# Kernel optimization log

Measured on AMD Instinct MI355X. Metric: run time of the kernel, lower is better.

Reference implementation:

```python
import jax, jax.numpy as jnp
import numpy as np

K = 5      # kernel_size
STRIDE = 1
EPS = 1e-7


def _extract_patches(x, k, s):
    # x: [B,H,W,C] -> [B,Ho,Wo,k,k,C], same (kh,kw,c) layout as tf.extract_image_patches VALID
    B, H, W, C = x.shape
    Ho = (H - k) // s + 1
    Wo = (W - k) // s + 1
    r = (jnp.arange(Ho) * s)[:, None] + jnp.arange(k)   # [Ho,k]
    c = (jnp.arange(Wo) * s)[:, None] + jnp.arange(k)   # [Wo,k]
    return x[:, r[:, None, :, None], c[None, :, None, :], :]


def _rotate(pflat, angle, k):
    # Replicates tf.contrib.image.transform with angles_to_projective_transforms,
    # including the (1+1e-7) normalization of the 3x3 matrix in the original code.
    # pflat: [N, k*k, C], angle: [N]; bilinear sampling, fill value 0 outside.
    N = pflat.shape[0]
    f32 = pflat.dtype
    co, si = jnp.cos(angle), jnp.sin(angle)
    km1 = jnp.asarray(k - 1, f32)
    xoff = (km1 - (co * km1 - si * km1)) * 0.5
    yoff = (km1 - (si * km1 + co * km1)) * 0.5
    scale = 1.0 / (1.0 + EPS)  # transforms /= transforms[:, 8:9] + 1e-7
    gy, gx = jnp.meshgrid(jnp.arange(k, dtype=f32), jnp.arange(k, dtype=f32), indexing='ij')
    sx = (co[:, None, None] * gx - si[:, None, None] * gy + xoff[:, None, None]) * scale
    sy = (si[:, None, None] * gx + co[:, None, None] * gy + yoff[:, None, None]) * scale
    sx = sx.reshape(N, k * k)
    sy = sy.reshape(N, k * k)
    x0 = jnp.floor(sx)
    y0 = jnp.floor(sy)
    wx = (sx - x0)[..., None]
    wy = (sy - y0)[..., None]
    x0i = x0.astype(jnp.int32)
    y0i = y0.astype(jnp.int32)

    def samp(yi, xi):
        valid = (xi >= 0) & (xi < k) & (yi >= 0) & (yi < k)
        idx = jnp.clip(yi, 0, k - 1) * k + jnp.clip(xi, 0, k - 1)   # [N,k*k]
        v = jnp.take_along_axis(pflat, idx[..., None], axis=1)      # [N,k*k,C]
        return jnp.where(valid[..., None], v, jnp.zeros((), f32))

    v00 = samp(y0i, x0i)
    v01 = samp(y0i, x0i + 1)
    v10 = samp(y0i + 1, x0i)
    v11 = samp(y0i + 1, x0i + 1)
    top = v00 * (1 - wx) + v01 * wx
    bot = v10 * (1 - wx) + v11 * wx
    return top * (1 - wy) + bot * wy   # [N,k*k,C]


def _forward(input_tensor, W, b):
    k, s = K, STRIDE
    B, H, Wd, C = input_tensor.shape
    patches = _extract_patches(input_tensor, k, s)      # [B,Ho,Wo,k,k,C]
    Ho, Wo = patches.shape[1], patches.shape[2]
    inten = patches.sum(-1)                             # [B,Ho,Wo,k,k] channel-sum intensity
    ridx = jnp.arange(k, dtype=patches.dtype)
    tot = inten.sum((-2, -1)) + EPS
    cr = (inten * ridx[:, None]).sum((-2, -1)) / tot    # centroid row
    cc = (inten * ridx[None, :]).sum((-2, -1)) / tot    # centroid col
    m = (k - 1) / 2.0                                   # meanCenter (same for row/col)
    angle = jnp.arctan2(cr - m, cc - m + EPS)           # [B,Ho,Wo]
    pflat = patches.reshape(B * Ho * Wo, k * k, C)
    rot = _rotate(pflat, angle.reshape(-1), k)          # [N,k*k,C]
    rot = rot.reshape(B, Ho * Wo, k * k * C)
    wflat = W.reshape(W.shape[0], -1)                   # [F, k*k*C]
    out = jnp.einsum('bpd,fd->bpf', rot, wflat)         # elementwise-mult-sum 'conv'
    return out.reshape(B, Ho, Wo, -1) + b


def setup_inputs():
    key = jax.random.key(0)
    k1, k2 = jax.random.split(key, 2)
    B, H, Wd, C, F = 4, 128, 128, 16, 32
    input_tensor = jax.random.uniform(k1, (B, H, Wd, C), dtype=jnp.float32)
    lim = float(np.sqrt(6.0 / (K * K * C + F)))  # glorot_uniform
    W = jax.random.uniform(k2, (F, K, K, C), minval=-lim, maxval=lim, dtype=jnp.float32)
    b = jnp.zeros((F,), jnp.float32)
    return {"input_tensor": input_tensor, "W": W, "b": b}


def reference(input_tensor, W, b):
    return _forward(input_tensor, W, b)
```

## Files before the change

### kernel.cpp

```cpp
#include <hip/hip_runtime.h>


#define KS     5
#define TILE   8
#define TW     (TILE + KS - 1)
#define SINH   24
#define C_IN   16
#define F_OUT  32
#define H_IN   128
#define W_IN   128
#define HO     124
#define WO     124
#define NBATCH 4
#define EPSF   1e-7f
#define BLOCK  256
#define KW     400

#define PART_OFF    6912
#define ANG_OFF     9216
#define RED_STRIDE  34
#define RED_WAVE    (64 * RED_STRIDE)
#define SMEM_BYTES  34816

typedef _Float16 half8  __attribute__((ext_vector_type(8)));
typedef _Float16 half4v __attribute__((ext_vector_type(4)));
typedef __attribute__((ext_vector_type(4))) float floatx4;

static __device__ __forceinline__ half8 blend8h(
    const _Float16* __restrict__ s_inh, int lxq, int lyq,
    float co, float si, float xo, float yo, int t, int ch0)
{
    const float scl = 1.0f / (1.0f + EPSF);
    int ky = t / KS, kx = t - KS * ky;
    float sx = (co * (float)kx - si * (float)ky + xo) * scl;
    float sy = (si * (float)kx + co * (float)ky + yo) * scl;
    float fx0 = floorf(sx), fy0 = floorf(sy);
    float wx = sx - fx0, wy = sy - fy0;
    int x0 = (int)fx0, y0 = (int)fy0;
    int x1 = x0 + 1, y1 = y0 + 1;
    float vx0 = (x0 >= 0 && x0 < KS) ? 1.f : 0.f;
    float vx1 = (x1 >= 0 && x1 < KS) ? 1.f : 0.f;
    float vy0 = (y0 >= 0 && y0 < KS) ? 1.f : 0.f;
    float vy1 = (y1 >= 0 && y1 < KS) ? 1.f : 0.f;
    float w00 = (1.f - wx) * (1.f - wy) * vx0 * vy0;
    float w01 = wx * (1.f - wy) * vx1 * vy0;
    float w10 = (1.f - wx) * wy * vx0 * vy1;
    float w11 = wx * wy * vx1 * vy1;
    int cx0 = min(max(x0, 0), KS - 1), cx1 = min(max(x1, 0), KS - 1);
    int cy0 = min(max(y0, 0), KS - 1), cy1 = min(max(y1, 0), KS - 1);
    const _Float16* p00 = &s_inh[((lyq + cy0) * TW + (lxq + cx0)) * SINH + ch0];
    const _Float16* p01 = &s_inh[((lyq + cy0) * TW + (lxq + cx1)) * SINH + ch0];
    const _Float16* p10 = &s_inh[((lyq + cy1) * TW + (lxq + cx0)) * SINH + ch0];
    const _Float16* p11 = &s_inh[((lyq + cy1) * TW + (lxq + cx1)) * SINH + ch0];
    half8 a = *(const half8*)p00;
    half8 b = *(const half8*)p01;
    half8 c = *(const half8*)p10;
    half8 d = *(const half8*)p11;
    _Float16 h00 = (_Float16)w00, h01 = (_Float16)w01;
    _Float16 h10 = (_Float16)w10, h11 = (_Float16)w11;
    half8 W00 = {h00,h00,h00,h00,h00,h00,h00,h00};
    half8 W01 = {h01,h01,h01,h01,h01,h01,h01,h01};
    half8 W10 = {h10,h10,h10,h10,h10,h10,h10,h10};
    half8 W11 = {h11,h11,h11,h11,h11,h11,h11,h11};
    return a * W00 + b * W01 + c * W10 + d * W11;
}

__global__ __launch_bounds__(BLOCK, 2) void rotconv_kernel(
    const float* __restrict__ in, const float* __restrict__ Wg,
    const float* __restrict__ bg, float* __restrict__ out)
{
    __shared__ __align__(16) char smem[SMEM_BYTES];
    _Float16* s_inh  = (_Float16*)smem;
    float*    s_part = (float*)(smem + PART_OFF);
    float4*   s_ang4 = (float4*)(smem + ANG_OFF);
    float*    red    = (float*)smem;

    const int tid  = threadIdx.x;
    const int bx = blockIdx.x, by = blockIdx.y, bimg = blockIdx.z;
    const int ox = bx * TILE, oy = by * TILE;

    const float* inb = in + (size_t)bimg * (H_IN * W_IN * C_IN);
    for (int i = tid; i < TW * TW * (C_IN / 4); i += BLOCK) {
        int cv = i & 3;
        int pp = i >> 2;
        int x = pp % TW, y = pp / TW;
        int gy = oy + y, gx = ox + x;
        float4 v = make_float4(0.f, 0.f, 0.f, 0.f);
        if (gy < H_IN && gx < W_IN)
            v = *(const float4*)(inb + ((size_t)(gy * W_IN + gx) * C_IN) + 4 * cv);
        half4v h = {(_Float16)v.x, (_Float16)v.y, (_Float16)v.z, (_Float16)v.w};
        *(half4v*)(&s_inh[pp * SINH + 4 * cv]) = h;
        s_part[pp * 4 + cv] = (v.x + v.y) + (v.z + v.w);
    }
    __syncthreads();

    if (tid < 64) {
        const int alx = tid & 7, aly = tid >> 3;
        float tot = EPSF, cr = 0.f, cc = 0.f;
        #pragma unroll
        for (int dy = 0; dy < KS; ++dy)
            #pragma unroll
            for (int dx = 0; dx < KS; ++dx) {
                float4 pv = *(const float4*)(&s_part[((aly + dy) * TW + (alx + dx)) * 4]);
                float v = (pv.x + pv.y) + (pv.z + pv.w);
                tot += v; cr += v * (float)dy; cc += v * (float)dx;
            }
        cr /= tot; cc /= tot;
        float dyv = cr - 2.0f, dxv = cc - 2.0f + EPSF;
        float r = sqrtf(dxv * dxv + dyv * dyv);
        float co, si;
        if (r < 1e-20f) { co = 1.f; si = 0.f; }
        else           { float ri = 1.0f / r; co = dxv * ri; si = dyv * ri; }
        float xoff = (4.0f - (co * 4.0f - si * 4.0f)) * 0.5f;
        float yoff = (4.0f - (si * 4.0f + co * 4.0f)) * 0.5f;
        s_ang4[tid] = make_float4(co, si, xoff, yoff);
    }
    __syncthreads();

    const int p    = tid & 63;
    const int wv   = tid >> 6;
    const int col  = p & 15;
    const int quad = p >> 4;

    float4 angs[4];
    #pragma unroll
    for (int m = 0; m < 4; ++m) angs[m] = s_ang4[16 * m + col];

    floatx4 acc[4][2];
    #pragma unroll
    for (int m = 0; m < 4; ++m) {
        acc[m][0] = (floatx4){0.f, 0.f, 0.f, 0.f};
        acc[m][1] = acc[m][0];
    }

    const int nstep = (wv == 0) ? 4 : 3;
    const int lxq = col & 7, lyq0 = col >> 3;
    const int ch0 = (quad & 1) * 8;
    const half8 zero8 = {0,0,0,0,0,0,0,0};

    #pragma unroll
    for (int s = 0; s < 4; ++s) {
        if (s < nstep) {
            const int ta = wv + 8 * s;
            const int tb = ta + 4;
            const int tq = (quad < 2) ? ta : tb;

            half8 bf0 = zero8, bf1 = zero8;
            if (tq < KS * KS) {
                const float* wp0 = Wg + (size_t)col * KW + tq * 16 + ch0;
                float4 a = *(const float4*)(wp0);
                float4 b = *(const float4*)(wp0 + 4);
                bf0 = (half8){(_Float16)a.x, (_Float16)a.y, (_Float16)a.z, (_Float16)a.w,
                              (_Float16)b.x, (_Float16)b.y, (_Float16)b.z, (_Float16)b.w};
                const float* wp1 = wp0 + (size_t)16 * KW;
                float4 c = *(const float4*)(wp1);
                float4 d = *(const float4*)(wp1 + 4);
                bf1 = (half8){(_Float16)c.x, (_Float16)c.y, (_Float16)c.z, (_Float16)c.w,
                              (_Float16)d.x, (_Float16)d.y, (_Float16)d.z, (_Float16)d.w};
            }

            #pragma unroll
            for (int m = 0; m < 4; ++m) {
                half8 av = zero8;
                if (tq < KS * KS)
                    av = blend8h(s_inh, lxq, 2 * m + lyq0,
                                 angs[m].x, angs[m].y, angs[m].z, angs[m].w,
                                 tq, ch0);
                acc[m][0] = __builtin_amdgcn_mfma_f32_16x16x32_f16(av, bf0, acc[m][0], 0, 0, 0);
                acc[m][1] = __builtin_amdgcn_mfma_f32_16x16x32_f16(av, bf1, acc[m][1], 0, 0, 0);
            }
        }
    }

    __syncthreads();
    #pragma unroll
    for (int m = 0; m < 4; ++m)
        #pragma unroll
        for (int n = 0; n < 2; ++n)
            #pragma unroll
            for (int r = 0; r < 4; ++r) {
                int px = 16 * m + 4 * quad + r;
                red[wv * RED_WAVE + px * RED_STRIDE + n * 16 + col] = acc[m][n][r];
            }
    __syncthreads();

    const int rpx = tid >> 2;
    const int rf0 = (tid & 3) * 8;
    float sum[8];
    #pragma unroll
    for (int j = 0; j < 8; ++j) sum[j] = bg[rf0 + j];
    #pragma unroll
    for (int w = 0; w < 4; ++w) {
        const float* rp = red + w * RED_WAVE + rpx * RED_STRIDE + rf0;
        #pragma unroll
        for (int j = 0; j < 8; ++j) sum[j] += rp[j];
    }
    const int ho = oy + (rpx >> 3), wo = ox + (rpx & 7);
    if (ho < HO && wo < WO) {
        float* op = out + (((size_t)bimg * HO + ho) * WO + wo) * F_OUT + rf0;
        *(float4*)op       = make_float4(sum[0], sum[1], sum[2], sum[3]);
        *(float4*)(op + 4) = make_float4(sum[4], sum[5], sum[6], sum[7]);
    }
}

extern "C" void kernel_launch(void* const* d_in, const int* in_sizes, int n_in,
                              void* d_out, int out_size, void* d_ws, size_t ws_size,
                              hipStream_t stream) {
    const float* in = (const float*)d_in[0];
    const float* Wg = (const float*)d_in[1];
    const float* bg = (const float*)d_in[2];
    float* out      = (float*)d_out;
    dim3 grid((WO + TILE - 1) / TILE, (HO + TILE - 1) / TILE, NBATCH);
    rotconv_kernel<<<grid, dim3(BLOCK), 0, stream>>>(in, Wg, bg, out);
}
```

Baseline: 71.43 us.

## Split output pixels across waves instead of K-reduction, drop LDS reduction

Each wave now owns 16 output pixels and iterates over all 25 taps itself. The old scheme had each wave accumulate a slice of the tap dimension for all 64 pixels, then reduced the partial sums across waves through shared memory. Removing that reduction removes two barriers and a large shared-memory buffer, so shared memory drops from 34816 to 10240 bytes and the occupancy hint rises to 4 blocks per CU. Each wave now runs 13 serial MFMA pairs on one accumulator pair, which gives less instruction-level parallelism, and weights are reloaded per step. Output is written with scalar strided stores instead of float4 stores.

New measurement: 75.78 us. 1.06x slower.

```diff
diff --git a/kernel.cpp b/kernel.cpp
--- a/kernel.cpp
+++ b/kernel.cpp
@@ -18,9 +18,7 @@
 
 #define PART_OFF    6912
 #define ANG_OFF     9216
-#define RED_STRIDE  34
-#define RED_WAVE    (64 * RED_STRIDE)
-#define SMEM_BYTES  34816
+#define SMEM_BYTES  10240
 
 typedef _Float16 half8  __attribute__((ext_vector_type(8)));
 typedef _Float16 half4v __attribute__((ext_vector_type(4)));
@@ -65,7 +63,7 @@
     return a * W00 + b * W01 + c * W10 + d * W11;
 }
 
-__global__ __launch_bounds__(BLOCK, 2) void rotconv_kernel(
+__global__ __launch_bounds__(BLOCK, 4) void rotconv_kernel(
     const float* __restrict__ in, const float* __restrict__ Wg,
     const float* __restrict__ bg, float* __restrict__ out)
 {
@@ -73,7 +71,6 @@
     _Float16* s_inh  = (_Float16*)smem;
     float*    s_part = (float*)(smem + PART_OFF);
     float4*   s_ang4 = (float4*)(smem + ANG_OFF);
-    float*    red    = (float*)smem;
 
     const int tid  = threadIdx.x;
     const int bx = blockIdx.x, by = blockIdx.y, bimg = blockIdx.z;
@@ -121,85 +118,52 @@
     const int wv   = tid >> 6;
     const int col  = p & 15;
     const int quad = p >> 4;
+    const int ch0  = (quad & 1) * 8;
 
-    float4 angs[4];
-    #pragma unroll
-    for (int m = 0; m < 4; ++m) angs[m] = s_ang4[16 * m + col];
+    const int lxq = col & 7;
+    const int lyq = 2 * wv + (col >> 3);
+    const float4 ang = s_ang4[16 * wv + col];
 
-    floatx4 acc[4][2];
-    #pragma unroll
-    for (int m = 0; m < 4; ++m) {
-        acc[m][0] = (floatx4){0.f, 0.f, 0.f, 0.f};
-        acc[m][1] = acc[m][0];
+    floatx4 acc0, acc1;
+    {
+        float bv0 = bg[col], bv1 = bg[col + 16];
+        acc0 = (floatx4){bv0, bv0, bv0, bv0};
+        acc1 = (floatx4){bv1, bv1, bv1, bv1};
     }
 
-    const int nstep = (wv == 0) ? 4 : 3;
-    const int lxq = col & 7, lyq0 = col >> 3;
-    const int ch0 = (quad & 1) * 8;
     const half8 zero8 = {0,0,0,0,0,0,0,0};
 
-    #pragma unroll
-    for (int s = 0; s < 4; ++s) {
-        if (s < nstep) {
-            const int ta = wv + 8 * s;
-            const int tb = ta + 4;
-            const int tq = (quad < 2) ? ta : tb;
+    for (int c = 0; c < 13; ++c) {
+        const int tq = 2 * c + (quad >> 1);
+        const bool val = (tq < KS * KS);
 
-            half8 bf0 = zero8, bf1 = zero8;
-            if (tq < KS * KS) {
-                const float* wp0 = Wg + (size_t)col * KW + tq * 16 + ch0;
-                float4 a = *(const float4*)(wp0);
-                float4 b = *(const float4*)(wp0 + 4);
-                bf0 = (half8){(_Float16)a.x, (_Float16)a.y, (_Float16)a.z, (_Float16)a.w,
-                              (_Float16)b.x, (_Float16)b.y, (_Float16)b.z, (_Float16)b.w};
-                const float* wp1 = wp0 + (size_t)16 * KW;
-                float4 c = *(const float4*)(wp1);
-                float4 d = *(const float4*)(wp1 + 4);
-                bf1 = (half8){(_Float16)c.x, (_Float16)c.y, (_Float16)c.z, (_Float16)c.w,
-                              (_Float16)d.x, (_Float16)d.y, (_Float16)d.z, (_Float16)d.w};
-            }
-
-            #pragma unroll
-            for (int m = 0; m < 4; ++m) {
-                half8 av = zero8;
-                if (tq < KS * KS)
-                    av = blend8h(s_inh, lxq, 2 * m + lyq0,
-                                 angs[m].x, angs[m].y, angs[m].z, angs[m].w,
-                                 tq, ch0);
-                acc[m][0] = __builtin_amdgcn_mfma_f32_16x16x32_f16(av, bf0, acc[m][0], 0, 0, 0);
-                acc[m][1] = __builtin_amdgcn_mfma_f32_16x16x32_f16(av, bf1, acc[m][1], 0, 0, 0);
-            }
+        half8 bf0 = zero8, bf1 = zero8, av = zero8;
+        if (val) {
+            const float* wp0 = Wg + (size_t)col * KW + tq * 16 + ch0;
+            float4 a = *(const float4*)(wp0);
+            float4 b = *(const float4*)(wp0 + 4);
+            bf0 = (half8){(_Float16)a.x, (_Float16)a.y, (_Float16)a.z, (_Float16)a.w,
+                          (_Float16)b.x, (_Float16)b.y, (_Float16)b.z, (_Float16)b.w};
+            const float* wp1 = wp0 + (size_t)16 * KW;
+            float4 cc4 = *(const float4*)(wp1);
+            float4 d4  = *(const float4*)(wp1 + 4);
+            bf1 = (half8){(_Float16)cc4.x, (_Float16)cc4.y, (_Float16)cc4.z, (_Float16)cc4.w,
+                          (_Float16)d4.x,  (_Float16)d4.y,  (_Float16)d4.z,  (_Float16)d4.w};
+            av = blend8h(s_inh, lxq, lyq, ang.x, ang.y, ang.z, ang.w, tq, ch0);
         }
+        acc0 = __builtin_amdgcn_mfma_f32_16x16x32_f16(av, bf0, acc0, 0, 0, 0);
+        acc1 = __builtin_amdgcn_mfma_f32_16x16x32_f16(av, bf1, acc1, 0, 0, 0);
     }
 
-    __syncthreads();
     #pragma unroll
-    for (int m = 0; m < 4; ++m)
-        #pragma unroll
-        for (int n = 0; n < 2; ++n)
-            #pragma unroll
-            for (int r = 0; r < 4; ++r) {
-                int px = 16 * m + 4 * quad + r;
-                red[wv * RED_WAVE + px * RED_STRIDE + n * 16 + col] = acc[m][n][r];
-            }
-    __syncthreads();
-
-    const int rpx = tid >> 2;
-    const int rf0 = (tid & 3) * 8;
-    float sum[8];
-    #pragma unroll
-    for (int j = 0; j < 8; ++j) sum[j] = bg[rf0 + j];
-    #pragma unroll
-    for (int w = 0; w < 4; ++w) {
-        const float* rp = red + w * RED_WAVE + rpx * RED_STRIDE + rf0;
-        #pragma unroll
-        for (int j = 0; j < 8; ++j) sum[j] += rp[j];
-    }
-    const int ho = oy + (rpx >> 3), wo = ox + (rpx & 7);
-    if (ho < HO && wo < WO) {
-        float* op = out + (((size_t)bimg * HO + ho) * WO + wo) * F_OUT + rf0;
-        *(float4*)op       = make_float4(sum[0], sum[1], sum[2], sum[3]);
-        *(float4*)(op + 4) = make_float4(sum[4], sum[5], sum[6], sum[7]);
+    for (int r = 0; r < 4; ++r) {
+        const int pix = 16 * wv + 4 * quad + r;
+        const int ho = oy + (pix >> 3), wo = ox + (pix & 7);
+        if (ho < HO && wo < WO) {
+            float* op = out + (((size_t)bimg * HO + ho) * WO + wo) * F_OUT + col;
+            op[0]  = acc0[r];
+            op[16] = acc1[r];
+        }
     }
 }
 
```
